# Performance work log

Measured on AMD Instinct MI355X. Metric: run time of the kernel, lower is better.

## Reference

```python
import jax, jax.numpy as jnp
import numpy as np

B, S, E, H, D = 2, 2048, 512, 8, 64
NEG = -1e10


def setup_inputs() -> dict:
    key = jax.random.key(0)
    k1, k2, k3, k4, k5, k6 = jax.random.split(key, 6)
    inputs = jax.random.normal(k1, (B, S, E), dtype=jnp.float32)
    keys = jax.random.normal(k2, (B, S, H, D), dtype=jnp.float32)
    values = jax.random.normal(k3, (B, S, H, D), dtype=jnp.float32)
    # xavier-uniform style scale for square weights
    lim = float(np.sqrt(6.0 / (E + H * D)))
    query_weights = jax.random.uniform(k4, (E, H * D), minval=-lim, maxval=lim, dtype=jnp.float32)
    output_weights = jax.random.uniform(k5, (H * D, E), minval=-lim, maxval=lim, dtype=jnp.float32)
    mask = jax.random.randint(k6, (B, S, S), 0, 2).astype(jnp.bool_)
    return {"inputs": inputs, "keys": keys, "values": values,
            "query_weights": query_weights, "output_weights": output_weights,
            "mask": mask}


def reference(inputs, keys, values, query_weights, output_weights, mask):
    # project queries: (B,S,E) @ (E,H*D) -> (B,S,H,D)
    q = jnp.matmul(inputs, query_weights).reshape(B, S, H, D)
    # scores: (B,H,Sq,Sk)
    scores = jnp.einsum('bqhd,bkhd->bhqk', q, keys) / jnp.sqrt(jnp.float32(D))
    # masked_fill(mask, -1e10); mask broadcasts over heads
    scores = jnp.where(mask[:, None, :, :], jnp.float32(NEG), scores)
    probs = jax.nn.softmax(scores, axis=-1)
    # (B,H,Sq,Sk) x (B,Sk,H,D) -> (B,Sq,H,D)
    out = jnp.einsum('bhqk,bkhd->bqhd', probs, values)
    out = out.reshape(B, S, H * D)
    return jnp.matmul(out, output_weights)
```

## Files before the change

kernel.cpp:

```cpp
#include <hip/hip_runtime.h>
#include <hip/hip_bf16.h>

namespace {

constexpr int B = 2, S = 2048, E = 512, H = 8, D = 64, HD = 512;
constexpr float SL = 0.125f * 1.44269504f;
constexpr int PLD = 40;

typedef __attribute__((ext_vector_type(8))) short bf16x8;
typedef __attribute__((ext_vector_type(4))) unsigned short u16x4;
typedef __attribute__((ext_vector_type(4))) float f32x4;
typedef __attribute__((ext_vector_type(4))) float float4v;

__device__ __forceinline__ ushort f2b(float x) {
  __hip_bfloat16 h = __float2bfloat16(x);
  return *reinterpret_cast<const ushort*>(&h);
}

__global__ __launch_bounds__(256) void prep_fused_kernel(
    const float* __restrict__ K, const float* __restrict__ V,
    const float* __restrict__ Wq, const float* __restrict__ Wo,
    const int* __restrict__ maskp,
    ushort* __restrict__ Kbf, ushort* __restrict__ Vtbf,
    ushort* __restrict__ Wtq, ushort* __restrict__ Wto,
    uint4* __restrict__ keep4) {
  const int bid = blockIdx.x;
  const int t = threadIdx.x;
  if (bid < 512) {
    __shared__ __align__(16) ushort Vn[64][76];
    const int kt = bid & 31;
    const int bh = bid >> 5;
    const int b = bh >> 3, h = bh & 7;
    const int k0 = kt * 64;
#pragma unroll
    for (int i = 0; i < 4; ++i) {
      int c = i * 256 + t;
      int kk = c >> 4, d4 = (c & 15) * 4;
      size_t g = ((size_t)(b * 2048 + k0 + kk) * 8 + h) * 64 + d4;
      float4v kv = *(const float4v*)(K + g);
      float4v vv = *(const float4v*)(V + g);
      u16x4 kp = {f2b(kv.x), f2b(kv.y), f2b(kv.z), f2b(kv.w)};
      u16x4 vp = {f2b(vv.x), f2b(vv.y), f2b(vv.z), f2b(vv.w)};
      *(u16x4*)(Kbf + ((size_t)(bh * 2048 + k0 + kk)) * 64 + d4) = kp;
      *(u16x4*)&Vn[kk][d4] = vp;
    }
    __syncthreads();
#pragma unroll
    for (int i = 0; i < 2; ++i) {
      int c = i * 256 + t;
      int kc8 = (c & 7) * 8, d = c >> 3;
      union { ushort u[8]; bf16x8 v; } p;
#pragma unroll
      for (int j = 0; j < 8; ++j) p.u[j] = Vn[kc8 + j][d];
      *(bf16x8*)(Vtbf + ((size_t)(bh * 64 + d)) * 2048 + k0 + kc8) = p.v;
    }
  } else if (bid < 640) {
    __shared__ __align__(16) ushort T[64][68];
    const int idx = bid - 512;
    const float* Wsrc = (idx >> 6) ? Wo : Wq;
    ushort* Wdst = (idx >> 6) ? Wto : Wtq;
    const int x = idx & 63;
    const int k0 = (x & 7) * 64, n0 = (x >> 3) * 64;
#pragma unroll
    for (int i = 0; i < 4; ++i) {
      int c = i * 256 + t;
      int kk = c >> 4, n4 = (c & 15) * 4;
      float4v v = *(const float4v*)(Wsrc + (size_t)(k0 + kk) * 512 + n0 + n4);
      u16x4 p = {f2b(v.x), f2b(v.y), f2b(v.z), f2b(v.w)};
      *(u16x4*)&T[kk][n4] = p;
    }
    __syncthreads();
#pragma unroll
    for (int i = 0; i < 2; ++i) {
      int c = i * 256 + t;
      int n = c >> 3, k8 = (c & 7) * 8;
      union { ushort u[8]; bf16x8 v; } p;
#pragma unroll
      for (int j = 0; j < 8; ++j) p.u[j] = T[k8 + j][n];
      *(bf16x8*)(Wdst + (size_t)(n0 + n) * 512 + k0 + k8) = p.v;
    }
  } else {
    const int wid = (bid - 640) * 4 + (t >> 6);
    const int row = wid >> 3, c = wid & 7;
    const int lane = t & 63;
    const int4 v = *((const int4*)(maskp + (size_t)row * 2048 + c * 256) + lane);
    unsigned long long bx = __ballot(v.x == 0);
    unsigned long long by = __ballot(v.y == 0);
    unsigned long long bz = __ballot(v.z == 0);
    unsigned long long bw = __ballot(v.w == 0);
    if (lane == 0)
      keep4[(size_t)row * 16 + c * 2] = uint4{(uint)bx, (uint)by, (uint)bz, (uint)bw};
    if (lane == 32)
      keep4[(size_t)row * 16 + c * 2 + 1] =
          uint4{(uint)(bx >> 32), (uint)(by >> 32), (uint)(bz >> 32), (uint)(bw >> 32)};
  }
}

__global__ __launch_bounds__(256) void proj_q_kernel(
    const float* __restrict__ A, const ushort* __restrict__ Wt, ushort* __restrict__ Qbf) {
  __shared__ __align__(16) ushort As[64][PLD];
  __shared__ __align__(16) ushort Ws[64][PLD];

  const int tid = threadIdx.x;
  const int lane = tid & 63;
  const int w = tid >> 6;
  const int col = lane & 15;
  const int quad = lane >> 4;
  const int m0 = blockIdx.y * 64;
  const int n0 = blockIdx.x * 64;
  const int wm = (w & 1) * 32;
  const int wn = (w >> 1) * 32;
  const int ar = tid >> 2;
  const int ak = (tid & 3) * 8;
  const int wn2 = tid >> 2;
  const int wkc = (tid & 3) * 8;

  f32x4 acc[2][2];
#pragma unroll
  for (int i = 0; i < 2; ++i)
#pragma unroll
    for (int j = 0; j < 2; ++j) acc[i][j] = f32x4{0.f, 0.f, 0.f, 0.f};

  const float* Ap = A + (size_t)(m0 + ar) * 512 + ak;
  const ushort* Wp = Wt + (size_t)(n0 + wn2) * 512 + wkc;
  float4v a0p = *(const float4v*)Ap;
  float4v a1p = *(const float4v*)(Ap + 4);
  bf16x8 wp = *(const bf16x8*)Wp;

  for (int kt = 0; kt < 16; ++kt) {
    if (kt) __syncthreads();
    {
      union { ushort u[8]; bf16x8 v; } ap;
      ap.u[0] = f2b(a0p.x); ap.u[1] = f2b(a0p.y); ap.u[2] = f2b(a0p.z); ap.u[3] = f2b(a0p.w);
      ap.u[4] = f2b(a1p.x); ap.u[5] = f2b(a1p.y); ap.u[6] = f2b(a1p.z); ap.u[7] = f2b(a1p.w);
      *(bf16x8*)&As[ar][ak] = ap.v;
      *(bf16x8*)&Ws[wn2][wkc] = wp;
    }
    if (kt < 15) {
      const int k1 = (kt + 1) * 32;
      a0p = *(const float4v*)(Ap + k1);
      a1p = *(const float4v*)(Ap + k1 + 4);
      wp = *(const bf16x8*)(Wp + k1);
    }
    __syncthreads();

    bf16x8 ah[2], wb[2];
#pragma unroll
    for (int i = 0; i < 2; ++i)
      ah[i] = *(const bf16x8*)&As[wm + i * 16 + col][quad * 8];
#pragma unroll
    for (int j = 0; j < 2; ++j)
      wb[j] = *(const bf16x8*)&Ws[wn + j * 16 + col][quad * 8];
#pragma unroll
    for (int i = 0; i < 2; ++i)
#pragma unroll
      for (int j = 0; j < 2; ++j)
        acc[i][j] = __builtin_amdgcn_mfma_f32_16x16x32_bf16(ah[i], wb[j], acc[i][j], 0, 0, 0);
  }

#pragma unroll
  for (int i = 0; i < 2; ++i)
#pragma unroll
    for (int j = 0; j < 2; ++j)
#pragma unroll
      for (int r = 0; r < 4; ++r) {
        int m = m0 + wm + i * 16 + (quad << 2) + r;
        int n = n0 + wn + j * 16 + col;
        int b = m >> 11, q = m & 2047, h = n >> 6, dd = n & 63;
        Qbf[((size_t)(b * 8 + h) * 2048 + q) * 64 + dd] = f2b(acc[i][j][r]);
      }
}

__global__ __launch_bounds__(256) void proj_out_kernel(
    const ushort* __restrict__ A, const ushort* __restrict__ Wt, float* __restrict__ C) {
  __shared__ __align__(16) ushort As[64][PLD];
  __shared__ __align__(16) ushort Ws[64][PLD];

  const int tid = threadIdx.x;
  const int lane = tid & 63;
  const int w = tid >> 6;
  const int col = lane & 15;
  const int quad = lane >> 4;
  const int m0 = blockIdx.y * 64;
  const int n0 = blockIdx.x * 64;
  const int wm = (w & 1) * 32;
  const int wn = (w >> 1) * 32;
  const int ar = tid >> 2;
  const int ak = (tid & 3) * 8;
  const int wn2 = tid >> 2;
  const int wkc = (tid & 3) * 8;

  f32x4 acc[2][2];
#pragma unroll
  for (int i = 0; i < 2; ++i)
#pragma unroll
    for (int j = 0; j < 2; ++j) acc[i][j] = f32x4{0.f, 0.f, 0.f, 0.f};

  const ushort* Ap = A + (size_t)(m0 + ar) * 512 + ak;
  const ushort* Wp = Wt + (size_t)(n0 + wn2) * 512 + wkc;
  bf16x8 apre = *(const bf16x8*)Ap;
  bf16x8 wp = *(const bf16x8*)Wp;

  for (int kt = 0; kt < 16; ++kt) {
    if (kt) __syncthreads();
    *(bf16x8*)&As[ar][ak] = apre;
    *(bf16x8*)&Ws[wn2][wkc] = wp;
    if (kt < 15) {
      const int k1 = (kt + 1) * 32;
      apre = *(const bf16x8*)(Ap + k1);
      wp = *(const bf16x8*)(Wp + k1);
    }
    __syncthreads();

    bf16x8 ah[2], wb[2];
#pragma unroll
    for (int i = 0; i < 2; ++i)
      ah[i] = *(const bf16x8*)&As[wm + i * 16 + col][quad * 8];
#pragma unroll
    for (int j = 0; j < 2; ++j)
      wb[j] = *(const bf16x8*)&Ws[wn + j * 16 + col][quad * 8];
#pragma unroll
    for (int i = 0; i < 2; ++i)
#pragma unroll
      for (int j = 0; j < 2; ++j)
        acc[i][j] = __builtin_amdgcn_mfma_f32_16x16x32_bf16(ah[i], wb[j], acc[i][j], 0, 0, 0);
  }

#pragma unroll
  for (int i = 0; i < 2; ++i)
#pragma unroll
    for (int j = 0; j < 2; ++j)
#pragma unroll
      for (int r = 0; r < 4; ++r)
        C[(size_t)(m0 + wm + i * 16 + (quad << 2) + r) * 512 + n0 + wn + j * 16 + col] =
            acc[i][j][r];
}

__global__ __launch_bounds__(256) void flash_attn_kernel(
    const ushort* __restrict__ Qbf, const ushort* __restrict__ Kbf,
    const ushort* __restrict__ Vtbf, const uint4* __restrict__ keep4,
    ushort* __restrict__ Op) {
  __shared__ __align__(16) ushort Ks[128][72];
  __shared__ __align__(16) ushort Vt[64][136];
  __shared__ __align__(16) ushort PQ[64][136];

  const int bid = blockIdx.x;
  const int qt = bid & 31;
  const int bh = bid >> 5;
  const int b = bh >> 3, h = bh & 7;
  const int q0 = qt * 64;
  const int tid = threadIdx.x, lane = tid & 63, w = tid >> 6;
  const int col = lane & 15, quad = lane >> 4, quad4 = quad * 4;

  const ushort* Qt = Qbf + (size_t)(bh * 2048 + q0) * 64;
#pragma unroll
  for (int i = 0; i < 2; ++i) {
    int c = i * 256 + tid;
    *(bf16x8*)&PQ[c >> 3][(c & 7) * 8] = *(const bf16x8*)(Qt + c * 8);
  }
  __syncthreads();
  const bf16x8 qb0 = *(const bf16x8*)&PQ[w * 16 + col][quad * 8];
  const bf16x8 qb1 = *(const bf16x8*)&PQ[w * 16 + col][32 + quad * 8];
  __syncthreads();

  f32x4 oacc[4];
#pragma unroll
  for (int c = 0; c < 4; ++c) oacc[c] = f32x4{0.f, 0.f, 0.f, 0.f};
  f32x4 lacc = f32x4{0.f, 0.f, 0.f, 0.f};

  union { ushort u[8]; bf16x8 v; } onesu;
#pragma unroll
  for (int j = 0; j < 8; ++j) onesu.u[j] = 0x3F80;
  const bf16x8 onesB = onesu.v;

  const uint4* kr = keep4 + (size_t)(b * 2048 + q0 + w * 16 + col) * 16;
  const ushort* Kbase = Kbf + (size_t)bh * 2048 * 64;
  const ushort* Vbase = Vtbf + (size_t)bh * 64 * 2048;

  bf16x8 kpre[4], vpre[4];
  uint4 kw = kr[0];
#pragma unroll
  for (int i = 0; i < 4; ++i) {
    int c = i * 256 + tid;
    kpre[i] = *(const bf16x8*)(Kbase + (size_t)c * 8);
    int d = c >> 4, k8 = (c & 15) * 8;
    vpre[i] = *(const bf16x8*)(Vbase + (size_t)d * 2048 + k8);
  }

  for (int kt = 0; kt < 16; ++kt) {
    if (kt) __syncthreads();
#pragma unroll
    for (int i = 0; i < 4; ++i) {
      int c = i * 256 + tid;
      *(bf16x8*)&Ks[c >> 3][(c & 7) * 8] = kpre[i];
      int d = c >> 4, k8 = (c & 15) * 8;
      *(bf16x8*)&Vt[d][k8] = vpre[i];
    }
    uint4 kwn = kw;
    if (kt < 15) {
      const int k1 = (kt + 1) * 128;
      kwn = kr[kt + 1];
#pragma unroll
      for (int i = 0; i < 4; ++i) {
        int c = i * 256 + tid;
        kpre[i] = *(const bf16x8*)(Kbase + (size_t)k1 * 64 + c * 8);
        int d = c >> 4, k8 = (c & 15) * 8;
        vpre[i] = *(const bf16x8*)(Vbase + (size_t)d * 2048 + k1 + k8);
      }
    }
    __syncthreads();

    f32x4 sc[8];
#pragma unroll
    for (int t = 0; t < 8; ++t) sc[t] = f32x4{0.f, 0.f, 0.f, 0.f};
#pragma unroll
    for (int t = 0; t < 8; ++t) {
      bf16x8 ka0 = *(const bf16x8*)&Ks[t * 16 + col][quad * 8];
      bf16x8 ka1 = *(const bf16x8*)&Ks[t * 16 + col][32 + quad * 8];
      sc[t] = __builtin_amdgcn_mfma_f32_16x16x32_bf16(ka0, qb0, sc[t], 0, 0, 0);
      sc[t] = __builtin_amdgcn_mfma_f32_16x16x32_bf16(ka1, qb1, sc[t], 0, 0, 0);
    }

    const uint mx_ = kw.x >> quad, my_ = kw.y >> quad, mz_ = kw.z >> quad, mw_ = kw.w >> quad;
#pragma unroll
    for (int t = 0; t < 8; ++t) {
      const int sh = 4 * t;
      float p0 = ((mx_ >> sh) & 1u) ? exp2f(sc[t][0] * SL) : 0.f;
      float p1 = ((my_ >> sh) & 1u) ? exp2f(sc[t][1] * SL) : 0.f;
      float p2 = ((mz_ >> sh) & 1u) ? exp2f(sc[t][2] * SL) : 0.f;
      float p3 = ((mw_ >> sh) & 1u) ? exp2f(sc[t][3] * SL) : 0.f;
      __hip_bfloat162 lo = __float22bfloat162_rn(float2{p0, p1});
      __hip_bfloat162 hi = __float22bfloat162_rn(float2{p2, p3});
      union { __hip_bfloat162 b2[2]; u16x4 v; } pk;
      pk.b2[0] = lo; pk.b2[1] = hi;
      *(u16x4*)&PQ[w * 16 + col][t * 16 + quad4] = pk.v;
    }
    __threadfence_block();

    bf16x8 pa[4];
#pragma unroll
    for (int kb = 0; kb < 4; ++kb)
      pa[kb] = *(const bf16x8*)&PQ[w * 16 + col][kb * 32 + quad * 8];
#pragma unroll
    for (int kb = 0; kb < 4; ++kb) {
      lacc = __builtin_amdgcn_mfma_f32_16x16x32_bf16(pa[kb], onesB, lacc, 0, 0, 0);
#pragma unroll
      for (int c = 0; c < 4; ++c) {
        bf16x8 vb = *(const bf16x8*)&Vt[c * 16 + col][kb * 32 + quad * 8];
        oacc[c] = __builtin_amdgcn_mfma_f32_16x16x32_bf16(pa[kb], vb, oacc[c], 0, 0, 0);
      }
    }
    kw = kwn;
  }

  float invO[4];
#pragma unroll
  for (int r = 0; r < 4; ++r) invO[r] = 1.f / lacc[r];
#pragma unroll
  for (int c = 0; c < 4; ++c)
#pragma unroll
    for (int r = 0; r < 4; ++r)
      Op[(size_t)(b * S + q0 + w * 16 + quad4 + r) * HD + h * D + c * 16 + col] =
          f2b(oacc[c][r] * invO[r]);
}

}

extern "C" void kernel_launch(void* const* d_in, const int* in_sizes, int n_in,
                              void* d_out, int out_size, void* d_ws, size_t ws_size,
                              hipStream_t stream) {
  const float* inputs = (const float*)d_in[0];
  const float* keys   = (const float*)d_in[1];
  const float* values = (const float*)d_in[2];
  const float* wq     = (const float*)d_in[3];
  const float* wo     = (const float*)d_in[4];
  const int*   maskp  = (const int*)d_in[5];
  float* out = (float*)d_out;

  ushort* Kbf  = (ushort*)d_out;
  ushort* Vtbf = Kbf + (size_t)2097152;

  char* ws = (char*)d_ws;
  ushort* Qbf   = (ushort*)ws;
  ushort* attnb = (ushort*)(ws + (4 << 20));
  uint4*  keep4 = (uint4*)(ws + (8 << 20));
  ushort* Wtq   = (ushort*)(ws + (9 << 20));
  ushort* Wto   = (ushort*)(ws + (9 << 20) + (512 << 10));

  dim3 blk(256);
  prep_fused_kernel<<<dim3(8832), blk, 0, stream>>>(keys, values, wq, wo, maskp,
                                                    Kbf, Vtbf, Wtq, Wto, keep4);
  proj_q_kernel<<<dim3(8, 64), blk, 0, stream>>>(inputs, Wtq, Qbf);
  flash_attn_kernel<<<dim3(512), blk, 0, stream>>>(Qbf, Kbf, Vtbf, keep4, attnb);
  proj_out_kernel<<<dim3(8, 64), blk, 0, stream>>>(attnb, Wto, out);
}
```

Baseline: 169.1 us.

## Fuse query projection into flash attention kernel prologue

Removes the separate proj_q kernel. Each attention block now computes its own 64x64 Q tile from the fp32 inputs and the bf16 transposed Wq, using the PQ shared buffer as staging. This drops one launch and the Q round trip through global memory. In exchange, the prologue of each attention block gets longer, with 16 k-steps and two syncs each.

```diff
diff --git a/kernel.cpp b/kernel.cpp
--- a/kernel.cpp
+++ b/kernel.cpp
@@ -96,8 +96,8 @@
   }
 }
 
-__global__ __launch_bounds__(256) void proj_q_kernel(
-    const float* __restrict__ A, const ushort* __restrict__ Wt, ushort* __restrict__ Qbf) {
+__global__ __launch_bounds__(256) void proj_out_kernel(
+    const ushort* __restrict__ A, const ushort* __restrict__ Wt, float* __restrict__ C) {
   __shared__ __align__(16) ushort As[64][PLD];
   __shared__ __align__(16) ushort Ws[64][PLD];
 
@@ -121,81 +121,6 @@
 #pragma unroll
     for (int j = 0; j < 2; ++j) acc[i][j] = f32x4{0.f, 0.f, 0.f, 0.f};
 
-  const float* Ap = A + (size_t)(m0 + ar) * 512 + ak;
-  const ushort* Wp = Wt + (size_t)(n0 + wn2) * 512 + wkc;
-  float4v a0p = *(const float4v*)Ap;
-  float4v a1p = *(const float4v*)(Ap + 4);
-  bf16x8 wp = *(const bf16x8*)Wp;
-
-  for (int kt = 0; kt < 16; ++kt) {
-    if (kt) __syncthreads();
-    {
-      union { ushort u[8]; bf16x8 v; } ap;
-      ap.u[0] = f2b(a0p.x); ap.u[1] = f2b(a0p.y); ap.u[2] = f2b(a0p.z); ap.u[3] = f2b(a0p.w);
-      ap.u[4] = f2b(a1p.x); ap.u[5] = f2b(a1p.y); ap.u[6] = f2b(a1p.z); ap.u[7] = f2b(a1p.w);
-      *(bf16x8*)&As[ar][ak] = ap.v;
-      *(bf16x8*)&Ws[wn2][wkc] = wp;
-    }
-    if (kt < 15) {
-      const int k1 = (kt + 1) * 32;
-      a0p = *(const float4v*)(Ap + k1);
-      a1p = *(const float4v*)(Ap + k1 + 4);
-      wp = *(const bf16x8*)(Wp + k1);
-    }
-    __syncthreads();
-
-    bf16x8 ah[2], wb[2];
-#pragma unroll
-    for (int i = 0; i < 2; ++i)
-      ah[i] = *(const bf16x8*)&As[wm + i * 16 + col][quad * 8];
-#pragma unroll
-    for (int j = 0; j < 2; ++j)
-      wb[j] = *(const bf16x8*)&Ws[wn + j * 16 + col][quad * 8];
-#pragma unroll
-    for (int i = 0; i < 2; ++i)
-#pragma unroll
-      for (int j = 0; j < 2; ++j)
-        acc[i][j] = __builtin_amdgcn_mfma_f32_16x16x32_bf16(ah[i], wb[j], acc[i][j], 0, 0, 0);
-  }
-
-#pragma unroll
-  for (int i = 0; i < 2; ++i)
-#pragma unroll
-    for (int j = 0; j < 2; ++j)
-#pragma unroll
-      for (int r = 0; r < 4; ++r) {
-        int m = m0 + wm + i * 16 + (quad << 2) + r;
-        int n = n0 + wn + j * 16 + col;
-        int b = m >> 11, q = m & 2047, h = n >> 6, dd = n & 63;
-        Qbf[((size_t)(b * 8 + h) * 2048 + q) * 64 + dd] = f2b(acc[i][j][r]);
-      }
-}
-
-__global__ __launch_bounds__(256) void proj_out_kernel(
-    const ushort* __restrict__ A, const ushort* __restrict__ Wt, float* __restrict__ C) {
-  __shared__ __align__(16) ushort As[64][PLD];
-  __shared__ __align__(16) ushort Ws[64][PLD];
-
-  const int tid = threadIdx.x;
-  const int lane = tid & 63;
-  const int w = tid >> 6;
-  const int col = lane & 15;
-  const int quad = lane >> 4;
-  const int m0 = blockIdx.y * 64;
-  const int n0 = blockIdx.x * 64;
-  const int wm = (w & 1) * 32;
-  const int wn = (w >> 1) * 32;
-  const int ar = tid >> 2;
-  const int ak = (tid & 3) * 8;
-  const int wn2 = tid >> 2;
-  const int wkc = (tid & 3) * 8;
-
-  f32x4 acc[2][2];
-#pragma unroll
-  for (int i = 0; i < 2; ++i)
-#pragma unroll
-    for (int j = 0; j < 2; ++j) acc[i][j] = f32x4{0.f, 0.f, 0.f, 0.f};
-
   const ushort* Ap = A + (size_t)(m0 + ar) * 512 + ak;
   const ushort* Wp = Wt + (size_t)(n0 + wn2) * 512 + wkc;
   bf16x8 apre = *(const bf16x8*)Ap;
@@ -237,9 +162,9 @@
 }
 
 __global__ __launch_bounds__(256) void flash_attn_kernel(
-    const ushort* __restrict__ Qbf, const ushort* __restrict__ Kbf,
-    const ushort* __restrict__ Vtbf, const uint4* __restrict__ keep4,
-    ushort* __restrict__ Op) {
+    const float* __restrict__ inp, const ushort* __restrict__ Wtq,
+    const ushort* __restrict__ Kbf, const ushort* __restrict__ Vtbf,
+    const uint4* __restrict__ keep4, ushort* __restrict__ Op) {
   __shared__ __align__(16) ushort Ks[128][72];
   __shared__ __align__(16) ushort Vt[64][136];
   __shared__ __align__(16) ushort PQ[64][136];
@@ -251,14 +176,67 @@
   const int q0 = qt * 64;
   const int tid = threadIdx.x, lane = tid & 63, w = tid >> 6;
   const int col = lane & 15, quad = lane >> 4, quad4 = quad * 4;
-
-  const ushort* Qt = Qbf + (size_t)(bh * 2048 + q0) * 64;
-#pragma unroll
-  for (int i = 0; i < 2; ++i) {
-    int c = i * 256 + tid;
-    *(bf16x8*)&PQ[c >> 3][(c & 7) * 8] = *(const bf16x8*)(Qt + c * 8);
-  }
-  __syncthreads();
+  const int wm = (w & 1) * 32;
+  const int wn = (w >> 1) * 32;
+
+  {
+    const int ar = tid >> 2;
+    const int ak = (tid & 3) * 8;
+
+    f32x4 qacc[2][2];
+#pragma unroll
+    for (int i = 0; i < 2; ++i)
+#pragma unroll
+      for (int j = 0; j < 2; ++j) qacc[i][j] = f32x4{0.f, 0.f, 0.f, 0.f};
+
+    const float* Ap = inp + (size_t)(b * 2048 + q0 + ar) * 512 + ak;
+    const ushort* Wp = Wtq + (size_t)(h * 64 + ar) * 512 + ak;
+    float4v a0p = *(const float4v*)Ap;
+    float4v a1p = *(const float4v*)(Ap + 4);
+    bf16x8 wp = *(const bf16x8*)Wp;
+
+    for (int kt = 0; kt < 16; ++kt) {
+      if (kt) __syncthreads();
+      {
+        union { ushort u[8]; bf16x8 v; } ap;
+        ap.u[0] = f2b(a0p.x); ap.u[1] = f2b(a0p.y); ap.u[2] = f2b(a0p.z); ap.u[3] = f2b(a0p.w);
+        ap.u[4] = f2b(a1p.x); ap.u[5] = f2b(a1p.y); ap.u[6] = f2b(a1p.z); ap.u[7] = f2b(a1p.w);
+        *(bf16x8*)&PQ[ar][ak] = ap.v;
+        *(bf16x8*)&PQ[ar][40 + ak] = wp;
+      }
+      if (kt < 15) {
+        const int k1 = (kt + 1) * 32;
+        a0p = *(const float4v*)(Ap + k1);
+        a1p = *(const float4v*)(Ap + k1 + 4);
+        wp = *(const bf16x8*)(Wp + k1);
+      }
+      __syncthreads();
+
+      bf16x8 ah[2], wb[2];
+#pragma unroll
+      for (int i = 0; i < 2; ++i)
+        ah[i] = *(const bf16x8*)&PQ[wm + i * 16 + col][quad * 8];
+#pragma unroll
+      for (int j = 0; j < 2; ++j)
+        wb[j] = *(const bf16x8*)&PQ[wn + j * 16 + col][40 + quad * 8];
+#pragma unroll
+      for (int i = 0; i < 2; ++i)
+#pragma unroll
+        for (int j = 0; j < 2; ++j)
+          qacc[i][j] = __builtin_amdgcn_mfma_f32_16x16x32_bf16(ah[i], wb[j], qacc[i][j], 0, 0, 0);
+    }
+
+    __syncthreads();
+#pragma unroll
+    for (int i = 0; i < 2; ++i)
+#pragma unroll
+      for (int j = 0; j < 2; ++j)
+#pragma unroll
+        for (int r = 0; r < 4; ++r)
+          PQ[wm + i * 16 + quad4 + r][wn + j * 16 + col] = f2b(qacc[i][j][r]);
+    __syncthreads();
+  }
+
   const bf16x8 qb0 = *(const bf16x8*)&PQ[w * 16 + col][quad * 8];
   const bf16x8 qb1 = *(const bf16x8*)&PQ[w * 16 + col][32 + quad * 8];
   __syncthreads();
@@ -381,16 +359,14 @@
   ushort* Vtbf = Kbf + (size_t)2097152;
 
   char* ws = (char*)d_ws;
-  ushort* Qbf   = (ushort*)ws;
-  ushort* attnb = (ushort*)(ws + (4 << 20));
-  uint4*  keep4 = (uint4*)(ws + (8 << 20));
-  ushort* Wtq   = (ushort*)(ws + (9 << 20));
-  ushort* Wto   = (ushort*)(ws + (9 << 20) + (512 << 10));
+  ushort* attnb = (ushort*)ws;
+  uint4*  keep4 = (uint4*)(ws + (4 << 20));
+  ushort* Wtq   = (ushort*)(ws + (5 << 20));
+  ushort* Wto   = (ushort*)(ws + (5 << 20) + (512 << 10));
 
   dim3 blk(256);
   prep_fused_kernel<<<dim3(8832), blk, 0, stream>>>(keys, values, wq, wo, maskp,
                                                     Kbf, Vtbf, Wtq, Wto, keep4);
-  proj_q_kernel<<<dim3(8, 64), blk, 0, stream>>>(inputs, Wtq, Qbf);
-  flash_attn_kernel<<<dim3(512), blk, 0, stream>>>(Qbf, Kbf, Vtbf, keep4, attnb);
+  flash_attn_kernel<<<dim3(512), blk, 0, stream>>>(inputs, Wtq, Kbf, Vtbf, keep4, attnb);
   proj_out_kernel<<<dim3(8, 64), blk, 0, stream>>>(attnb, Wto, out);
 }
```

Result: faster. 164.9 us (-2.5%).
